# Optimization experiments

Measured on AMD Instinct MI355X. Metric: run time of the kernel, lower is better.

Reference implementation:

```python
import jax, jax.numpy as jnp
import numpy as np

N = 512      # hidden states
M = 32000    # observation vocab
B = 64       # batch
TMAX = 256   # max sequence length


def setup_inputs() -> dict:
    key = jax.random.key(0)
    k1, k2, k3, k4, k5 = jax.random.split(key, 5)
    return {
        "x": jax.random.randint(k1, (B, TMAX), 0, M),          # observations
        "T": jax.random.randint(k2, (B,), 1, TMAX + 1),        # lengths in [1, TMAX]
        "trans": jax.random.normal(k3, (N, N), dtype=jnp.float32),  # unnormalized transition
        "emis": jax.random.normal(k4, (N, M), dtype=jnp.float32),   # unnormalized emission
        "prior": jax.random.normal(k5, (N,), dtype=jnp.float32),    # unnormalized state priors
    }


def reference(x, T, trans, emis, prior):
    # columns of transition matrix sum to 1 (log_softmax over dim=0 in torch)
    log_A = jax.nn.log_softmax(trans, axis=0)    # (N, N): log_A[j, k] = log p(z_t=j | z_{t-1}=k)
    log_E = jax.nn.log_softmax(emis, axis=1)     # (N, M)
    log_pi = jax.nn.log_softmax(prior, axis=0)   # (N,)

    # emission log-probs for every timestep, gathered once: (B, TMAX, N)
    em = log_E.T[x]

    alpha0 = em[:, 0, :] + log_pi                # (B, N)

    def step(alpha, em_t):
        # out[b, j] = em_t[b, j] + logsumexp_k (log_A[j, k] + alpha[b, k])
        new = em_t + jax.nn.logsumexp(alpha[:, None, :] + log_A[None, :, :], axis=2)
        return new, new

    _, alphas = jax.lax.scan(step, alpha0, jnp.swapaxes(em[:, 1:, :], 0, 1))  # (TMAX-1, B, N)
    log_alpha = jnp.concatenate([alpha0[:, None, :], jnp.swapaxes(alphas, 0, 1)], axis=1)  # (B, TMAX, N)

    log_sums = jax.nn.logsumexp(log_alpha, axis=2)                       # (B, TMAX)
    log_probs = jnp.take_along_axis(log_sums, (T - 1)[:, None], axis=1)  # (B, 1)
    return log_probs
```

## Files before the change

kernel.cpp:

```cpp
#include <hip/hip_runtime.h>
#include <math.h>

#define Nn 512
#define Mm 32000
#define Bb 64
#define Tt 256
#define NCONS 4
#define NPROD 128

typedef float v4f __attribute__((ext_vector_type(4)));
typedef float f4  __attribute__((ext_vector_type(4)));
typedef int   v4i __attribute__((ext_vector_type(4)));
typedef int   v8i __attribute__((ext_vector_type(8)));

__device__ inline int pk4fp8(float a, float b, float c, float d) {
  int r = __builtin_amdgcn_cvt_pk_fp8_f32(a, b, 0, false);
  r = __builtin_amdgcn_cvt_pk_fp8_f32(c, d, r, true);
  return r;
}

__global__ void k_colsum(const float* __restrict__ trans, float* __restrict__ colsum) {
  int tid = threadIdx.x;
  int j0 = blockIdx.x * 16;
  float a0 = 0.f, a1 = 0.f;
  for (int r = 0; r < 16; ++r) {
    a0 += __expf(trans[(j0 + r) * Nn + tid]);
    a1 += __expf(trans[(j0 + r) * Nn + 256 + tid]);
  }
  atomicAdd(&colsum[tid], a0);
  atomicAdd(&colsum[256 + tid], a1);
}

__global__ void k_writeA8(const float* __restrict__ trans, const float* __restrict__ colsum,
                          int* __restrict__ A8) {
  int d = blockIdx.x * 256 + threadIdx.x;
  int j = d >> 7, k0 = (d & 127) << 2;
  float v0 = 256.f * __expf(trans[j * Nn + k0 + 0]) / colsum[k0 + 0];
  float v1 = 256.f * __expf(trans[j * Nn + k0 + 1]) / colsum[k0 + 1];
  float v2 = 256.f * __expf(trans[j * Nn + k0 + 2]) / colsum[k0 + 2];
  float v3 = 256.f * __expf(trans[j * Nn + k0 + 3]) / colsum[k0 + 3];
  A8[d] = pk4fp8(v0, v1, v2, v3);
}

__global__ __launch_bounds__(512, 2) void k_fused(
    const char* __restrict__ A8, const float* __restrict__ emis,
    const int* __restrict__ x, const float* __restrict__ prior,
    const int* __restrict__ Tlen, float* __restrict__ Pem2,
    int* __restrict__ progress, float* __restrict__ out)
{
  __shared__ __align__(16) char ybuf[2][16 * Nn];
  __shared__ __align__(16) float Spart[2][16][12];
  __shared__ float ss[512];
  __shared__ float fac[2][4];
  const int tid = threadIdx.x;

  if (blockIdx.x >= NCONS) {
    const int p = blockIdx.x - NCONS;
    const int j0 = p * 4;
    float ps = __expf(prior[tid]);
    ss[tid] = ps; __syncthreads();
    for (int off = 256; off; off >>= 1) { if (tid < off) ss[tid] += ss[tid + off]; __syncthreads(); }
    float ptot = ss[0]; __syncthreads();
    for (int q = 0; q < 4; ++q) {
      const f4* row4 = (const f4*)(emis + (size_t)(j0 + q) * Mm);
      float s = 0.f;
      for (int i = tid; i < Mm / 4; i += 512) {
        f4 v = row4[i];
        s += __expf(v[0]) + __expf(v[1]) + __expf(v[2]) + __expf(v[3]);
      }
      ss[tid] = s; __syncthreads();
      for (int off = 256; off; off >>= 1) { if (tid < off) ss[tid] += ss[tid + off]; __syncthreads(); }
      if (tid == 0) {
        float rs = 32768.f / ss[0];
        fac[0][q] = rs;
        fac[1][q] = rs * 256.f * __expf(prior[j0 + q]) / ptot;
      }
      __syncthreads();
    }
    const float* r0 = emis + (size_t)(j0 + 0) * Mm;
    const float* r1 = emis + (size_t)(j0 + 1) * Mm;
    const float* r2 = emis + (size_t)(j0 + 2) * Mm;
    const float* r3 = emis + (size_t)(j0 + 3) * Mm;
    f4* P4 = (f4*)Pem2;
    for (int c8 = 0; c8 < 8; ++c8) {
      #pragma unroll
      for (int r = 0; r < 4; ++r) {
        int idx = c8 * 2048 + r * 512 + tid;
        int t = idx >> 6, b = idx & 63;
        int mv = x[b * Tt + t];
        const float* fq = (t == 0) ? &fac[1][0] : &fac[0][0];
        f4 o;
        o[0] = __expf(r0[mv]) * fq[0]; o[1] = __expf(r1[mv]) * fq[1];
        o[2] = __expf(r2[mv]) * fq[2]; o[3] = __expf(r3[mv]) * fq[3];
        P4[t * 8192 + (b >> 4) * 2048 + p * 16 + (b & 15)] = o;
      }
      __syncthreads();
      if (tid == 0) {
        __builtin_amdgcn_fence(__ATOMIC_RELEASE, "agent");
        __hip_atomic_fetch_add(&progress[c8], 1, __ATOMIC_RELAXED, __HIP_MEMORY_SCOPE_AGENT);
      }
    }
    return;
  }

  const int g = blockIdx.x;
  const int w = tid >> 6, lane = tid & 63;
  const int c = lane & 15, kq = lane >> 4;
  const int jw = w * 64;
  const int swz = (c & 7) << 4;
  const int b = g * 16 + c;

  v8i af[4][4];
  #pragma unroll
  for (int rt = 0; rt < 4; ++rt)
    #pragma unroll
    for (int kc = 0; kc < 4; ++kc)
      af[rt][kc] = *reinterpret_cast<const v8i*>(
          A8 + (size_t)(jw + rt * 16 + c) * Nn + kc * 128 + kq * 32);

  const int Tb = Tlen[b];
  int E = 23;
  int csafe = 0;

  #define ENSURE(NEED)                                                                      \
    while (csafe <= (NEED)) {                                                               \
      if (__hip_atomic_load(&progress[csafe], __ATOMIC_RELAXED,                             \
                            __HIP_MEMORY_SCOPE_AGENT) >= NPROD) {                           \
        ++csafe;                                                                            \
        __builtin_amdgcn_fence(__ATOMIC_ACQUIRE, "agent");                                  \
      } else __builtin_amdgcn_s_sleep(2);                                                   \
    }

  int roA[4], roB[4], wof[4];
  #pragma unroll
  for (int kc = 0; kc < 4; ++kc) {
    int base = c * Nn + kc * 128 + kq * 32;
    roA[kc] = base ^ swz;
    roB[kc] = (base + 16) ^ swz;
  }
  #pragma unroll
  for (int rt = 0; rt < 4; ++rt)
    wof[rt] = (c * Nn + jw + rt * 16 + kq * 4) ^ swz;
  char* const yb0 = &ybuf[0][0];

  if (tid < 192) ((float*)&Spart[0][0][0])[tid] = 0.f;
  __syncthreads();

  ENSURE(0);

  {
    int cc = tid & 15, grp = tid >> 4, jb = grp * 16, sz = (cc & 7) << 4;
    const f4* P0 = (const f4*)Pem2 + g * 2048 + (jb >> 2) * 16 + cc;
    float psum = 0.f;
    #pragma unroll
    for (int q = 0; q < 4; ++q) {
      f4 v = P0[q * 16];
      psum += (v[0] + v[1]) + (v[2] + v[3]);
      *reinterpret_cast<int*>(yb0 + ((cc * Nn + jb + q * 4) ^ sz)) = pk4fp8(v[0], v[1], v[2], v[3]);
    }
    atomicAdd(&Spart[0][cc][grp & 7], psum);
  }
  __syncthreads();

  const f4* PB = (const f4*)Pem2;
  #define PIDX(T, RT) ((T) * 8192 + g * 2048 + ((jw + (RT) * 16) >> 2) * 16 + kq * 16 + c)
  f4 pem[4];
  #pragma unroll
  for (int rt = 0; rt < 4; ++rt) pem[rt] = PB[PIDX(1, rt)];

  int pp = 0;
  for (int t = 1; t <= Tt; ++t) {
    int sp = pp >> 13;
    f4 s0 = *reinterpret_cast<const f4*>(&Spart[sp][c][0]);
    f4 s1 = *reinterpret_cast<const f4*>(&Spart[sp][c][4]);
    float S = ((s0[0] + s0[1]) + (s0[2] + s0[3])) + ((s1[0] + s1[1]) + (s1[2] + s1[3]));
    int expb = (int)((__float_as_uint(S) >> 23) & 0xFF);
    if (w == 0 && kq == 0 && Tb == t) out[b] = __logf(S) - (float)E * 0.69314718056f;
    if (t == Tt) break;
    E += 150 - expb;
    float scl = __uint_as_float((unsigned)(254 - expb) << 23);

    bool pf = (t + 1 < Tt);
    if (pf && (((t + 1) & 31) == 0)) ENSURE((t + 1) >> 5);
    f4 pemN[4];
    if (pf) {
      #pragma unroll
      for (int rt = 0; rt < 4; ++rt) pemN[rt] = PB[PIDX(t + 1, rt)];
    }

    const char* rp = yb0 + pp;
    union BU { v8i v; v4i h[2]; };
    BU bu[4];
    #pragma unroll
    for (int kc = 0; kc < 4; ++kc) {
      bu[kc].h[0] = *reinterpret_cast<const v4i*>(rp + roA[kc]);
      bu[kc].h[1] = *reinterpret_cast<const v4i*>(rp + roB[kc]);
    }

    v4f a0 = {0.f,0.f,0.f,0.f}, a1 = {0.f,0.f,0.f,0.f};
    v4f a2 = {0.f,0.f,0.f,0.f}, a3 = {0.f,0.f,0.f,0.f};
    #pragma unroll
    for (int kc = 0; kc < 4; ++kc) {
      v8i bbv = bu[kc].v;
      a0 = __builtin_amdgcn_mfma_scale_f32_16x16x128_f8f6f4(af[0][kc], bbv, a0, 0, 0, 0, 0x7F, 0, 0x7F);
      a1 = __builtin_amdgcn_mfma_scale_f32_16x16x128_f8f6f4(af[1][kc], bbv, a1, 0, 0, 0, 0x7F, 0, 0x7F);
      a2 = __builtin_amdgcn_mfma_scale_f32_16x16x128_f8f6f4(af[2][kc], bbv, a2, 0, 0, 0, 0x7F, 0, 0x7F);
      a3 = __builtin_amdgcn_mfma_scale_f32_16x16x128_f8f6f4(af[3][kc], bbv, a3, 0, 0, 0, 0x7F, 0, 0x7F);
    }

    char* wp = yb0 + (pp ^ 8192);
    float vsum = 0.f;
    #define EPI(AC, RT) {                                                     \
      float v0 = AC[0] * (pem[RT][0] * scl), v1 = AC[1] * (pem[RT][1] * scl); \
      float v2 = AC[2] * (pem[RT][2] * scl), v3 = AC[3] * (pem[RT][3] * scl); \
      vsum += (v0 + v1) + (v2 + v3);                                          \
      *reinterpret_cast<int*>(wp + wof[RT]) = pk4fp8(v0, v1, v2, v3); }
    EPI(a0, 0) EPI(a1, 1) EPI(a2, 2) EPI(a3, 3)
    #undef EPI

    vsum += __shfl_xor(vsum, 16);
    vsum += __shfl_xor(vsum, 32);
    if (kq == 0) Spart[sp ^ 1][c][w] = vsum;

    if (pf) {
      #pragma unroll
      for (int rt = 0; rt < 4; ++rt) pem[rt] = pemN[rt];
    }
    pp ^= 8192;
    __syncthreads();
  }
  #undef PIDX
  #undef ENSURE
}

extern "C" void kernel_launch(void* const* d_in, const int* in_sizes, int n_in,
                              void* d_out, int out_size, void* d_ws, size_t ws_size,
                              hipStream_t stream) {
  const int*   x     = (const int*)  d_in[0];
  const int*   Tlen  = (const int*)  d_in[1];
  const float* trans = (const float*)d_in[2];
  const float* emis  = (const float*)d_in[3];
  const float* prior = (const float*)d_in[4];
  float* out = (float*)d_out;

  char* w = (char*)d_ws;
  char*  A8       = (char*)(w);
  float* colsum   = (float*)(w + (512 << 10));
  int*   progress = (int*)  (w + (512 << 10) + 4096);
  float* Pem2     = (float*)(w + (1024 << 10));

  hipMemsetAsync(w + (512 << 10), 0, 8192, stream);
  k_colsum <<<32,        256, 0, stream>>>(trans, colsum);
  k_writeA8<<<256,       256, 0, stream>>>(trans, colsum, (int*)A8);
  k_fused  <<<NCONS + NPROD, 512, 0, stream>>>(A8, emis, x, prior, Tlen, Pem2, progress, out);
}
```

Baseline: 355.9 us.

## Fold transition normalization into fused kernel and batch emission row sums

Removes the two preprocessing kernels. The first 32 producer blocks now compute transition column sums and signal the consumers through a progress flag. The consumers then build their fp8 transition fragments directly from trans with the reciprocal column sums, instead of reading a precomputed A8 buffer. The producer emission normalization now reduces all four rows in one pass with a vector reduction, and a large LDS pad forces one block per CU. This cuts launch overhead and the A8 round trip, but puts extra exp work and a spin-wait on the consumer startup path.

```diff
diff --git a/kernel.cpp b/kernel.cpp
--- a/kernel.cpp
+++ b/kernel.cpp
@@ -19,64 +19,64 @@
   return r;
 }
 
-__global__ void k_colsum(const float* __restrict__ trans, float* __restrict__ colsum) {
-  int tid = threadIdx.x;
-  int j0 = blockIdx.x * 16;
-  float a0 = 0.f, a1 = 0.f;
-  for (int r = 0; r < 16; ++r) {
-    a0 += __expf(trans[(j0 + r) * Nn + tid]);
-    a1 += __expf(trans[(j0 + r) * Nn + 256 + tid]);
-  }
-  atomicAdd(&colsum[tid], a0);
-  atomicAdd(&colsum[256 + tid], a1);
-}
-
-__global__ void k_writeA8(const float* __restrict__ trans, const float* __restrict__ colsum,
-                          int* __restrict__ A8) {
-  int d = blockIdx.x * 256 + threadIdx.x;
-  int j = d >> 7, k0 = (d & 127) << 2;
-  float v0 = 256.f * __expf(trans[j * Nn + k0 + 0]) / colsum[k0 + 0];
-  float v1 = 256.f * __expf(trans[j * Nn + k0 + 1]) / colsum[k0 + 1];
-  float v2 = 256.f * __expf(trans[j * Nn + k0 + 2]) / colsum[k0 + 2];
-  float v3 = 256.f * __expf(trans[j * Nn + k0 + 3]) / colsum[k0 + 3];
-  A8[d] = pk4fp8(v0, v1, v2, v3);
-}
-
-__global__ __launch_bounds__(512, 2) void k_fused(
-    const char* __restrict__ A8, const float* __restrict__ emis,
+__global__ __launch_bounds__(512, 1) void k_all(
+    const float* __restrict__ trans, const float* __restrict__ emis,
     const int* __restrict__ x, const float* __restrict__ prior,
-    const int* __restrict__ Tlen, float* __restrict__ Pem2,
-    int* __restrict__ progress, float* __restrict__ out)
+    const int* __restrict__ Tlen, float* __restrict__ colsum,
+    float* __restrict__ Pem2, int* __restrict__ progress, float* __restrict__ out)
 {
   __shared__ __align__(16) char ybuf[2][16 * Nn];
   __shared__ __align__(16) float Spart[2][16][12];
-  __shared__ float ss[512];
-  __shared__ float fac[2][4];
+  __shared__ __align__(16) float ss[512];
+  __shared__ __align__(16) f4 ss4[512];
+  __shared__ char pad_[60 * 1024];
   const int tid = threadIdx.x;
+  if ((int)blockIdx.x == -1) ((volatile char*)pad_)[tid] = 1;
 
   if (blockIdx.x >= NCONS) {
     const int p = blockIdx.x - NCONS;
     const int j0 = p * 4;
-    float ps = __expf(prior[tid]);
-    ss[tid] = ps; __syncthreads();
+
+    if (p < 32) {
+      float a = 0.f;
+      #pragma unroll 4
+      for (int r = 0; r < 16; ++r)
+        a += __expf(trans[(p * 16 + r) * Nn + tid]);
+      atomicAdd(&colsum[tid], a);
+      __syncthreads();
+      if (tid == 0) {
+        __builtin_amdgcn_fence(__ATOMIC_RELEASE, "agent");
+        __hip_atomic_fetch_add(&progress[8], 1, __ATOMIC_RELAXED, __HIP_MEMORY_SCOPE_AGENT);
+      }
+    }
+
+    float e = __expf(prior[tid]);
+    ss[tid] = e; __syncthreads();
     for (int off = 256; off; off >>= 1) { if (tid < off) ss[tid] += ss[tid + off]; __syncthreads(); }
-    float ptot = ss[0]; __syncthreads();
+    const float ptot = ss[0];
+
+    const f4* q0 = (const f4*)(emis + (size_t)(j0 + 0) * Mm);
+    const f4* q1 = (const f4*)(emis + (size_t)(j0 + 1) * Mm);
+    const f4* q2 = (const f4*)(emis + (size_t)(j0 + 2) * Mm);
+    const f4* q3 = (const f4*)(emis + (size_t)(j0 + 3) * Mm);
+    f4 a4 = {0.f, 0.f, 0.f, 0.f};
+    for (int i = tid; i < Mm / 4; i += 512) {
+      f4 v0 = q0[i], v1 = q1[i], v2 = q2[i], v3 = q3[i];
+      a4[0] += (__expf(v0[0]) + __expf(v0[1])) + (__expf(v0[2]) + __expf(v0[3]));
+      a4[1] += (__expf(v1[0]) + __expf(v1[1])) + (__expf(v1[2]) + __expf(v1[3]));
+      a4[2] += (__expf(v2[0]) + __expf(v2[1])) + (__expf(v2[2]) + __expf(v2[3]));
+      a4[3] += (__expf(v3[0]) + __expf(v3[1])) + (__expf(v3[2]) + __expf(v3[3]));
+    }
+    ss4[tid] = a4; __syncthreads();
+    for (int off = 256; off; off >>= 1) { if (tid < off) ss4[tid] += ss4[tid + off]; __syncthreads(); }
+    f4 tot = ss4[0];
+    f4 rs, fz;
+    #pragma unroll
     for (int q = 0; q < 4; ++q) {
-      const f4* row4 = (const f4*)(emis + (size_t)(j0 + q) * Mm);
-      float s = 0.f;
-      for (int i = tid; i < Mm / 4; i += 512) {
-        f4 v = row4[i];
-        s += __expf(v[0]) + __expf(v[1]) + __expf(v[2]) + __expf(v[3]);
-      }
-      ss[tid] = s; __syncthreads();
-      for (int off = 256; off; off >>= 1) { if (tid < off) ss[tid] += ss[tid + off]; __syncthreads(); }
-      if (tid == 0) {
-        float rs = 32768.f / ss[0];
-        fac[0][q] = rs;
-        fac[1][q] = rs * 256.f * __expf(prior[j0 + q]) / ptot;
-      }
-      __syncthreads();
-    }
+      rs[q] = 32768.f / tot[q];
+      fz[q] = rs[q] * 256.f * __expf(prior[j0 + q]) / ptot;
+    }
+
     const float* r0 = emis + (size_t)(j0 + 0) * Mm;
     const float* r1 = emis + (size_t)(j0 + 1) * Mm;
     const float* r2 = emis + (size_t)(j0 + 2) * Mm;
@@ -88,10 +88,9 @@
         int idx = c8 * 2048 + r * 512 + tid;
         int t = idx >> 6, b = idx & 63;
         int mv = x[b * Tt + t];
-        const float* fq = (t == 0) ? &fac[1][0] : &fac[0][0];
-        f4 o;
-        o[0] = __expf(r0[mv]) * fq[0]; o[1] = __expf(r1[mv]) * fq[1];
-        o[2] = __expf(r2[mv]) * fq[2]; o[3] = __expf(r3[mv]) * fq[3];
+        f4 fq = (t == 0) ? fz : rs;
+        f4 o = { __expf(r0[mv]) * fq[0], __expf(r1[mv]) * fq[1],
+                 __expf(r2[mv]) * fq[2], __expf(r3[mv]) * fq[3] };
         P4[t * 8192 + (b >> 4) * 2048 + p * 16 + (b & 15)] = o;
       }
       __syncthreads();
@@ -110,13 +109,33 @@
   const int swz = (c & 7) << 4;
   const int b = g * 16 + c;
 
+  if (tid == 0) {
+    while (__hip_atomic_load(&progress[8], __ATOMIC_RELAXED, __HIP_MEMORY_SCOPE_AGENT) < 32)
+      __builtin_amdgcn_s_sleep(2);
+  }
+  __syncthreads();
+  __builtin_amdgcn_fence(__ATOMIC_ACQUIRE, "agent");
+  ss[tid] = 256.f / colsum[tid];
+  __syncthreads();
+
   v8i af[4][4];
   #pragma unroll
-  for (int rt = 0; rt < 4; ++rt)
-    #pragma unroll
-    for (int kc = 0; kc < 4; ++kc)
-      af[rt][kc] = *reinterpret_cast<const v8i*>(
-          A8 + (size_t)(jw + rt * 16 + c) * Nn + kc * 128 + kq * 32);
+  for (int rt = 0; rt < 4; ++rt) {
+    const float* trow = trans + (size_t)(jw + rt * 16 + c) * Nn;
+    #pragma unroll
+    for (int kc = 0; kc < 4; ++kc) {
+      int k0 = kc * 128 + kq * 32;
+      int wd[8];
+      #pragma unroll
+      for (int u = 0; u < 8; ++u) {
+        f4 tv = *(const f4*)(trow + k0 + u * 4);
+        f4 cw = *(const f4*)(&ss[k0 + u * 4]);
+        wd[u] = pk4fp8(__expf(tv[0]) * cw[0], __expf(tv[1]) * cw[1],
+                       __expf(tv[2]) * cw[2], __expf(tv[3]) * cw[3]);
+      }
+      af[rt][kc] = (v8i){wd[0], wd[1], wd[2], wd[3], wd[4], wd[5], wd[6], wd[7]};
+    }
+  }
 
   const int Tb = Tlen[b];
   int E = 23;
@@ -173,7 +192,8 @@
     int sp = pp >> 13;
     f4 s0 = *reinterpret_cast<const f4*>(&Spart[sp][c][0]);
     f4 s1 = *reinterpret_cast<const f4*>(&Spart[sp][c][4]);
-    float S = ((s0[0] + s0[1]) + (s0[2] + s0[3])) + ((s1[0] + s1[1]) + (s1[2] + s1[3]));
+    f4 st = s0 + s1;
+    float S = (st[0] + st[1]) + (st[2] + st[3]);
     int expb = (int)((__float_as_uint(S) >> 23) & 0xFF);
     if (w == 0 && kq == 0 && Tb == t) out[b] = __logf(S) - (float)E * 0.69314718056f;
     if (t == Tt) break;
@@ -208,16 +228,17 @@
       a3 = __builtin_amdgcn_mfma_scale_f32_16x16x128_f8f6f4(af[3][kc], bbv, a3, 0, 0, 0, 0x7F, 0, 0x7F);
     }
 
+    v4f scl4 = {scl, scl, scl, scl};
     char* wp = yb0 + (pp ^ 8192);
-    float vsum = 0.f;
-    #define EPI(AC, RT) {                                                     \
-      float v0 = AC[0] * (pem[RT][0] * scl), v1 = AC[1] * (pem[RT][1] * scl); \
-      float v2 = AC[2] * (pem[RT][2] * scl), v3 = AC[3] * (pem[RT][3] * scl); \
-      vsum += (v0 + v1) + (v2 + v3);                                          \
-      *reinterpret_cast<int*>(wp + wof[RT]) = pk4fp8(v0, v1, v2, v3); }
+    f4 vs4 = {0.f, 0.f, 0.f, 0.f};
+    #define EPI(AC, RT) {                                   \
+      v4f vv = AC * (pem[RT] * scl4);                       \
+      vs4 += vv;                                            \
+      *reinterpret_cast<int*>(wp + wof[RT]) = pk4fp8(vv[0], vv[1], vv[2], vv[3]); }
     EPI(a0, 0) EPI(a1, 1) EPI(a2, 2) EPI(a3, 3)
     #undef EPI
 
+    float vsum = (vs4[0] + vs4[1]) + (vs4[2] + vs4[3]);
     vsum += __shfl_xor(vsum, 16);
     vsum += __shfl_xor(vsum, 32);
     if (kq == 0) Spart[sp ^ 1][c][w] = vsum;
@@ -244,13 +265,11 @@
   float* out = (float*)d_out;
 
   char* w = (char*)d_ws;
-  char*  A8       = (char*)(w);
   float* colsum   = (float*)(w + (512 << 10));
   int*   progress = (int*)  (w + (512 << 10) + 4096);
   float* Pem2     = (float*)(w + (1024 << 10));
 
   hipMemsetAsync(w + (512 << 10), 0, 8192, stream);
-  k_colsum <<<32,        256, 0, stream>>>(trans, colsum);
-  k_writeA8<<<256,       256, 0, stream>>>(trans, colsum, (int*)A8);
-  k_fused  <<<NCONS + NPROD, 512, 0, stream>>>(A8, emis, x, prior, Tlen, Pem2, progress, out);
+  k_all<<<NCONS + NPROD, 512, 0, stream>>>(trans, emis, x, prior, Tlen,
+                                           colsum, Pem2, progress, out);
 }
```

Result: slower. 453.3 us (+27.4%).

## Double block size to 1024 threads, halving per-wave MFMA work in recurrence

Applied to the files above, without the earlier changes.

The fused kernel now launches with 1024 threads per block. In the four consumer blocks each wave owns 32 output rows instead of 64, so each recurrence step issues 8 MFMAs per wave instead of 16, spread across 16 waves. The producer blocks compute all four emission row sums in one fused loop with a single vector reduction instead of four serial reductions. The emission-factor prefetch for the next step is dropped: pem values are loaded inside the step that uses them. This shortens the per-step latency chain, at the cost of a wider barrier and a global load on the critical path each step.

```diff
diff --git a/kernel.cpp b/kernel.cpp
--- a/kernel.cpp
+++ b/kernel.cpp
@@ -42,41 +42,49 @@
   A8[d] = pk4fp8(v0, v1, v2, v3);
 }
 
-__global__ __launch_bounds__(512, 2) void k_fused(
+__global__ __launch_bounds__(1024, 4) void k_fused(
     const char* __restrict__ A8, const float* __restrict__ emis,
     const int* __restrict__ x, const float* __restrict__ prior,
     const int* __restrict__ Tlen, float* __restrict__ Pem2,
     int* __restrict__ progress, float* __restrict__ out)
 {
   __shared__ __align__(16) char ybuf[2][16 * Nn];
-  __shared__ __align__(16) float Spart[2][16][12];
-  __shared__ float ss[512];
-  __shared__ float fac[2][4];
+  __shared__ __align__(16) float Spart[2][16][20];
+  __shared__ __align__(16) float ss[1024];
+  __shared__ __align__(16) f4 ss4[1024];
   const int tid = threadIdx.x;
 
   if (blockIdx.x >= NCONS) {
     const int p = blockIdx.x - NCONS;
     const int j0 = p * 4;
-    float ps = __expf(prior[tid]);
-    ss[tid] = ps; __syncthreads();
-    for (int off = 256; off; off >>= 1) { if (tid < off) ss[tid] += ss[tid + off]; __syncthreads(); }
-    float ptot = ss[0]; __syncthreads();
+
+    float e = (tid < Nn) ? __expf(prior[tid]) : 0.f;
+    ss[tid] = e; __syncthreads();
+    for (int off = 512; off; off >>= 1) { if (tid < off) ss[tid] += ss[tid + off]; __syncthreads(); }
+    const float ptot = ss[0];
+
+    const f4* q0 = (const f4*)(emis + (size_t)(j0 + 0) * Mm);
+    const f4* q1 = (const f4*)(emis + (size_t)(j0 + 1) * Mm);
+    const f4* q2 = (const f4*)(emis + (size_t)(j0 + 2) * Mm);
+    const f4* q3 = (const f4*)(emis + (size_t)(j0 + 3) * Mm);
+    f4 a4 = {0.f, 0.f, 0.f, 0.f};
+    for (int i = tid; i < Mm / 4; i += 1024) {
+      f4 v0 = q0[i], v1 = q1[i], v2 = q2[i], v3 = q3[i];
+      a4[0] += (__expf(v0[0]) + __expf(v0[1])) + (__expf(v0[2]) + __expf(v0[3]));
+      a4[1] += (__expf(v1[0]) + __expf(v1[1])) + (__expf(v1[2]) + __expf(v1[3]));
+      a4[2] += (__expf(v2[0]) + __expf(v2[1])) + (__expf(v2[2]) + __expf(v2[3]));
+      a4[3] += (__expf(v3[0]) + __expf(v3[1])) + (__expf(v3[2]) + __expf(v3[3]));
+    }
+    ss4[tid] = a4; __syncthreads();
+    for (int off = 512; off; off >>= 1) { if (tid < off) ss4[tid] += ss4[tid + off]; __syncthreads(); }
+    f4 tot = ss4[0];
+    f4 rs, fz;
+    #pragma unroll
     for (int q = 0; q < 4; ++q) {
-      const f4* row4 = (const f4*)(emis + (size_t)(j0 + q) * Mm);
-      float s = 0.f;
-      for (int i = tid; i < Mm / 4; i += 512) {
-        f4 v = row4[i];
-        s += __expf(v[0]) + __expf(v[1]) + __expf(v[2]) + __expf(v[3]);
-      }
-      ss[tid] = s; __syncthreads();
-      for (int off = 256; off; off >>= 1) { if (tid < off) ss[tid] += ss[tid + off]; __syncthreads(); }
-      if (tid == 0) {
-        float rs = 32768.f / ss[0];
-        fac[0][q] = rs;
-        fac[1][q] = rs * 256.f * __expf(prior[j0 + q]) / ptot;
-      }
-      __syncthreads();
-    }
+      rs[q] = 32768.f / tot[q];
+      fz[q] = rs[q] * 256.f * __expf(prior[j0 + q]) / ptot;
+    }
+
     const float* r0 = emis + (size_t)(j0 + 0) * Mm;
     const float* r1 = emis + (size_t)(j0 + 1) * Mm;
     const float* r2 = emis + (size_t)(j0 + 2) * Mm;
@@ -84,14 +92,13 @@
     f4* P4 = (f4*)Pem2;
     for (int c8 = 0; c8 < 8; ++c8) {
       #pragma unroll
-      for (int r = 0; r < 4; ++r) {
-        int idx = c8 * 2048 + r * 512 + tid;
+      for (int r = 0; r < 2; ++r) {
+        int idx = c8 * 2048 + r * 1024 + tid;
         int t = idx >> 6, b = idx & 63;
         int mv = x[b * Tt + t];
-        const float* fq = (t == 0) ? &fac[1][0] : &fac[0][0];
-        f4 o;
-        o[0] = __expf(r0[mv]) * fq[0]; o[1] = __expf(r1[mv]) * fq[1];
-        o[2] = __expf(r2[mv]) * fq[2]; o[3] = __expf(r3[mv]) * fq[3];
+        f4 fq = (t == 0) ? fz : rs;
+        f4 o = { __expf(r0[mv]) * fq[0], __expf(r1[mv]) * fq[1],
+                 __expf(r2[mv]) * fq[2], __expf(r3[mv]) * fq[3] };
         P4[t * 8192 + (b >> 4) * 2048 + p * 16 + (b & 15)] = o;
       }
       __syncthreads();
@@ -106,13 +113,13 @@
   const int g = blockIdx.x;
   const int w = tid >> 6, lane = tid & 63;
   const int c = lane & 15, kq = lane >> 4;
-  const int jw = w * 64;
+  const int jw = w * 32;
   const int swz = (c & 7) << 4;
   const int b = g * 16 + c;
 
-  v8i af[4][4];
+  v8i af[2][4];
   #pragma unroll
-  for (int rt = 0; rt < 4; ++rt)
+  for (int rt = 0; rt < 2; ++rt)
     #pragma unroll
     for (int kc = 0; kc < 4; ++kc)
       af[rt][kc] = *reinterpret_cast<const v8i*>(
@@ -131,29 +138,23 @@
       } else __builtin_amdgcn_s_sleep(2);                                                   \
     }
 
-  int roA[4], roB[4], wof[4];
-  #pragma unroll
-  for (int kc = 0; kc < 4; ++kc) {
-    int base = c * Nn + kc * 128 + kq * 32;
-    roA[kc] = base ^ swz;
-    roB[kc] = (base + 16) ^ swz;
-  }
-  #pragma unroll
-  for (int rt = 0; rt < 4; ++rt)
-    wof[rt] = (c * Nn + jw + rt * 16 + kq * 4) ^ swz;
+  const int roA0 = (c * Nn + kq * 32) ^ swz;
+  const int roB0 = roA0 ^ 16;
+  const int wof0 = (c * Nn + jw + kq * 4) ^ swz;
+  const int wof1 = wof0 ^ 16;
   char* const yb0 = &ybuf[0][0];
 
-  if (tid < 192) ((float*)&Spart[0][0][0])[tid] = 0.f;
+  if (tid < 640) ((float*)&Spart[0][0][0])[tid] = 0.f;
   __syncthreads();
 
   ENSURE(0);
 
   {
-    int cc = tid & 15, grp = tid >> 4, jb = grp * 16, sz = (cc & 7) << 4;
+    int cc = tid & 15, grp = tid >> 4, jb = grp * 8, sz = (cc & 7) << 4;
     const f4* P0 = (const f4*)Pem2 + g * 2048 + (jb >> 2) * 16 + cc;
     float psum = 0.f;
     #pragma unroll
-    for (int q = 0; q < 4; ++q) {
+    for (int q = 0; q < 2; ++q) {
       f4 v = P0[q * 16];
       psum += (v[0] + v[1]) + (v[2] + v[3]);
       *reinterpret_cast<int*>(yb0 + ((cc * Nn + jb + q * 4) ^ sz)) = pk4fp8(v[0], v[1], v[2], v[3]);
@@ -164,68 +165,60 @@
 
   const f4* PB = (const f4*)Pem2;
   #define PIDX(T, RT) ((T) * 8192 + g * 2048 + ((jw + (RT) * 16) >> 2) * 16 + kq * 16 + c)
-  f4 pem[4];
-  #pragma unroll
-  for (int rt = 0; rt < 4; ++rt) pem[rt] = PB[PIDX(1, rt)];
 
   int pp = 0;
   for (int t = 1; t <= Tt; ++t) {
+    if (t < Tt && (t & 31) == 0) ENSURE(t >> 5);
+
+    f4 pem0, pem1;
+    if (t < Tt) { pem0 = PB[PIDX(t, 0)]; pem1 = PB[PIDX(t, 1)]; }
+
     int sp = pp >> 13;
     f4 s0 = *reinterpret_cast<const f4*>(&Spart[sp][c][0]);
     f4 s1 = *reinterpret_cast<const f4*>(&Spart[sp][c][4]);
-    float S = ((s0[0] + s0[1]) + (s0[2] + s0[3])) + ((s1[0] + s1[1]) + (s1[2] + s1[3]));
+    f4 s2 = *reinterpret_cast<const f4*>(&Spart[sp][c][8]);
+    f4 s3 = *reinterpret_cast<const f4*>(&Spart[sp][c][12]);
+    f4 st = (s0 + s1) + (s2 + s3);
+    float S = (st[0] + st[1]) + (st[2] + st[3]);
     int expb = (int)((__float_as_uint(S) >> 23) & 0xFF);
     if (w == 0 && kq == 0 && Tb == t) out[b] = __logf(S) - (float)E * 0.69314718056f;
     if (t == Tt) break;
     E += 150 - expb;
     float scl = __uint_as_float((unsigned)(254 - expb) << 23);
 
-    bool pf = (t + 1 < Tt);
-    if (pf && (((t + 1) & 31) == 0)) ENSURE((t + 1) >> 5);
-    f4 pemN[4];
-    if (pf) {
-      #pragma unroll
-      for (int rt = 0; rt < 4; ++rt) pemN[rt] = PB[PIDX(t + 1, rt)];
-    }
-
     const char* rp = yb0 + pp;
+    v4f a0 = {0.f,0.f,0.f,0.f}, a1 = {0.f,0.f,0.f,0.f};
     union BU { v8i v; v4i h[2]; };
-    BU bu[4];
-    #pragma unroll
-    for (int kc = 0; kc < 4; ++kc) {
-      bu[kc].h[0] = *reinterpret_cast<const v4i*>(rp + roA[kc]);
-      bu[kc].h[1] = *reinterpret_cast<const v4i*>(rp + roB[kc]);
-    }
-
-    v4f a0 = {0.f,0.f,0.f,0.f}, a1 = {0.f,0.f,0.f,0.f};
-    v4f a2 = {0.f,0.f,0.f,0.f}, a3 = {0.f,0.f,0.f,0.f};
-    #pragma unroll
-    for (int kc = 0; kc < 4; ++kc) {
-      v8i bbv = bu[kc].v;
-      a0 = __builtin_amdgcn_mfma_scale_f32_16x16x128_f8f6f4(af[0][kc], bbv, a0, 0, 0, 0, 0x7F, 0, 0x7F);
-      a1 = __builtin_amdgcn_mfma_scale_f32_16x16x128_f8f6f4(af[1][kc], bbv, a1, 0, 0, 0, 0x7F, 0, 0x7F);
-      a2 = __builtin_amdgcn_mfma_scale_f32_16x16x128_f8f6f4(af[2][kc], bbv, a2, 0, 0, 0, 0x7F, 0, 0x7F);
-      a3 = __builtin_amdgcn_mfma_scale_f32_16x16x128_f8f6f4(af[3][kc], bbv, a3, 0, 0, 0, 0x7F, 0, 0x7F);
-    }
-
+    BU bu0, bu1;
+    bu0.h[0] = *reinterpret_cast<const v4i*>(rp + roA0);
+    bu0.h[1] = *reinterpret_cast<const v4i*>(rp + roB0);
+    bu1.h[0] = *reinterpret_cast<const v4i*>(rp + roA0 + 128);
+    bu1.h[1] = *reinterpret_cast<const v4i*>(rp + roB0 + 128);
+    a0 = __builtin_amdgcn_mfma_scale_f32_16x16x128_f8f6f4(af[0][0], bu0.v, a0, 0, 0, 0, 0x7F, 0, 0x7F);
+    a1 = __builtin_amdgcn_mfma_scale_f32_16x16x128_f8f6f4(af[1][0], bu0.v, a1, 0, 0, 0, 0x7F, 0, 0x7F);
+    a0 = __builtin_amdgcn_mfma_scale_f32_16x16x128_f8f6f4(af[0][1], bu1.v, a0, 0, 0, 0, 0x7F, 0, 0x7F);
+    a1 = __builtin_amdgcn_mfma_scale_f32_16x16x128_f8f6f4(af[1][1], bu1.v, a1, 0, 0, 0, 0x7F, 0, 0x7F);
+    bu0.h[0] = *reinterpret_cast<const v4i*>(rp + roA0 + 256);
+    bu0.h[1] = *reinterpret_cast<const v4i*>(rp + roB0 + 256);
+    bu1.h[0] = *reinterpret_cast<const v4i*>(rp + roA0 + 384);
+    bu1.h[1] = *reinterpret_cast<const v4i*>(rp + roB0 + 384);
+    a0 = __builtin_amdgcn_mfma_scale_f32_16x16x128_f8f6f4(af[0][2], bu0.v, a0, 0, 0, 0, 0x7F, 0, 0x7F);
+    a1 = __builtin_amdgcn_mfma_scale_f32_16x16x128_f8f6f4(af[1][2], bu0.v, a1, 0, 0, 0, 0x7F, 0, 0x7F);
+    a0 = __builtin_amdgcn_mfma_scale_f32_16x16x128_f8f6f4(af[0][3], bu1.v, a0, 0, 0, 0, 0x7F, 0, 0x7F);
+    a1 = __builtin_amdgcn_mfma_scale_f32_16x16x128_f8f6f4(af[1][3], bu1.v, a1, 0, 0, 0, 0x7F, 0, 0x7F);
+
+    v4f scl4 = {scl, scl, scl, scl};
     char* wp = yb0 + (pp ^ 8192);
-    float vsum = 0.f;
-    #define EPI(AC, RT) {                                                     \
-      float v0 = AC[0] * (pem[RT][0] * scl), v1 = AC[1] * (pem[RT][1] * scl); \
-      float v2 = AC[2] * (pem[RT][2] * scl), v3 = AC[3] * (pem[RT][3] * scl); \
-      vsum += (v0 + v1) + (v2 + v3);                                          \
-      *reinterpret_cast<int*>(wp + wof[RT]) = pk4fp8(v0, v1, v2, v3); }
-    EPI(a0, 0) EPI(a1, 1) EPI(a2, 2) EPI(a3, 3)
-    #undef EPI
-
+    v4f v0 = a0 * (pem0 * scl4);
+    v4f v1 = a1 * (pem1 * scl4);
+    *reinterpret_cast<int*>(wp + wof0) = pk4fp8(v0[0], v0[1], v0[2], v0[3]);
+    *reinterpret_cast<int*>(wp + wof1) = pk4fp8(v1[0], v1[1], v1[2], v1[3]);
+    f4 vs4 = v0 + v1;
+    float vsum = (vs4[0] + vs4[1]) + (vs4[2] + vs4[3]);
     vsum += __shfl_xor(vsum, 16);
     vsum += __shfl_xor(vsum, 32);
     if (kq == 0) Spart[sp ^ 1][c][w] = vsum;
 
-    if (pf) {
-      #pragma unroll
-      for (int rt = 0; rt < 4; ++rt) pem[rt] = pemN[rt];
-    }
     pp ^= 8192;
     __syncthreads();
   }
@@ -250,7 +243,7 @@
   float* Pem2     = (float*)(w + (1024 << 10));
 
   hipMemsetAsync(w + (512 << 10), 0, 8192, stream);
-  k_colsum <<<32,        256, 0, stream>>>(trans, colsum);
-  k_writeA8<<<256,       256, 0, stream>>>(trans, colsum, (int*)A8);
-  k_fused  <<<NCONS + NPROD, 512, 0, stream>>>(A8, emis, x, prior, Tlen, Pem2, progress, out);
-}
+  k_colsum <<<32,  256, 0, stream>>>(trans, colsum);
+  k_writeA8<<<256, 256, 0, stream>>>(trans, colsum, (int*)A8);
+  k_fused  <<<NCONS + NPROD, 1024, 0, stream>>>(A8, emis, x, prior, Tlen, Pem2, progress, out);
+}
```

Result: no change. 351.9 us (-1.1%).
